# Kernel optimization log

Hardware: AMD Instinct MI355X
Metric: run time of the kernel (lower is better)

The kernel has to match this reference:

```python
import jax, jax.numpy as jnp
import numpy as np
from jax import lax

N, CI, CO, K, H, W_SP, M = 32, 256, 256, 3, 64, 64, 4
TAU = 1.0 / 30.0
PAD = 1  # spatial-preserving for k=3, stride=1, dilation=1


def setup_inputs() -> dict:
    key = jax.random.key(0)
    ks = jax.random.split(key, 6)
    # kaiming_normal fan_out for the kernel bank: fan_out = CO*K*K (per torch semantics on this 6D tensor layout)
    fan_out = CO * K * K
    std = np.sqrt(2.0 / fan_out)
    x = jax.random.normal(ks[0], (N, CI, H, W_SP), dtype=jnp.float32)
    Wbank = jax.random.normal(ks[1], (CO, M, CI, K, K), dtype=jnp.float32) * std
    Bbank = jnp.zeros((CO, M), dtype=jnp.float32)
    hid = CI // M  # att_fc hidden = in_channels // num_weights
    w1 = jax.random.normal(ks[2], (hid, CI), dtype=jnp.float32) * np.sqrt(1.0 / CI)
    b1 = jnp.zeros((hid,), dtype=jnp.float32)
    w2 = jax.random.normal(ks[3], (M, hid), dtype=jnp.float32) * np.sqrt(1.0 / hid)
    b2 = jnp.zeros((M,), dtype=jnp.float32)
    return {"x": x, "Wbank": Wbank, "Bbank": Bbank, "w1": w1, "b1": b1, "w2": w2, "b2": b2}


def reference(x, Wbank, Bbank, w1, b1, w2, b2):
    n, ci, h, w = x.shape
    co = Wbank.shape[0]
    # attention over kernels: global avg pool -> 1x1 conv MLP -> softmax(logits * tau)
    pooled = jnp.mean(x, axis=(2, 3))                      # N,Ci
    hmid = jax.nn.relu(pooled @ w1.T + b1)                 # N,hid
    logits = hmid @ w2.T + b2                              # N,M
    pi = jax.nn.softmax(logits * TAU, axis=1)              # N,M
    # per-sample aggregated kernels and biases
    wn = jnp.einsum("nm,omikl->noikl", pi, Wbank)          # N,Co,Ci,K,K
    bn = pi @ Bbank.T                                      # N,Co
    # batch-as-groups conv2d (spatial-preserving)
    xg = x.reshape(1, n * ci, h, w)
    wg = wn.reshape(n * co, ci, K, K)
    y = lax.conv_general_dilated(
        xg, wg,
        window_strides=(1, 1),
        padding=[(PAD, PAD), (PAD, PAD)],
        rhs_dilation=(1, 1),
        dimension_numbers=("NCHW", "OIHW", "NCHW"),
        feature_group_count=n,
    )
    y = y.reshape(n, co, h, w) + bn[:, :, None, None]
    return y
```

## Files before the change

kernel.cpp:

```cpp
#include <hip/hip_runtime.h>
#include <hip/hip_bf16.h>
#include <stdint.h>

typedef __bf16 bf16;
typedef __bf16 bf16x8 __attribute__((ext_vector_type(8)));
typedef float f32x4 __attribute__((ext_vector_type(4)));

#define TAU (1.0f/30.0f)

#define NB 32
#define CI 256
#define CO 256
#define HH 64
#define WW 64
#define HID 64

#define WN_ELEMS ((size_t)NB*8*9*16*512)
#define WN_BYTES (WN_ELEMS*2)
#define PLANE_E 34848
#define XB_ELEMS ((size_t)NB*32*PLANE_E)
#define XB_BYTES (XB_ELEMS*2)

__device__ __forceinline__ void async16(void* lds_uniform_base, const void* g_perlane) {
  __builtin_amdgcn_global_load_lds(
      (const __attribute__((address_space(1))) uint32_t*)g_perlane,
      (__attribute__((address_space(3))) uint32_t*)lds_uniform_base, 16, 0, 0);
}

__global__ void cvt_pool_kernel(const float* __restrict__ x, bf16* __restrict__ xb,
                                float* __restrict__ pooled) {
  const int cg = blockIdx.x, n = blockIdx.y, tid = threadIdx.x;
  const float* base = x + ((size_t)n*CI + cg*8)*4096;
  bf16* ob = xb + ((size_t)n*32 + cg)*PLANE_E;
  for (int i = tid; i < 260; i += 256) {
    int hr, wl;
    if (i < 66)       { hr = 0;       wl = i; }
    else if (i < 132) { hr = 65;      wl = i - 66; }
    else if (i < 196) { hr = i - 131; wl = 0; }
    else              { hr = i - 195; wl = 65; }
    *(int4*)(ob + ((size_t)hr*66 + wl)*8) = int4{0,0,0,0};
  }
  float s[8];
#pragma unroll
  for (int j = 0; j < 8; ++j) s[j] = 0.f;
  for (int it = 0; it < 16; ++it) {
    int pos = it*256 + tid;
    int h = pos >> 6, w = pos & 63;
    bf16x8 o;
#pragma unroll
    for (int j = 0; j < 8; ++j) {
      float v = base[(size_t)j*4096 + pos];
      s[j] += v;
      o[j] = (bf16)v;
    }
    *(bf16x8*)(ob + ((size_t)(h+1)*66 + (w+1))*8) = o;
  }
  __shared__ float red[4][8];
#pragma unroll
  for (int j = 0; j < 8; ++j)
#pragma unroll
    for (int off = 32; off; off >>= 1) s[j] += __shfl_xor(s[j], off);
  int wv = tid >> 6, lane = tid & 63;
  if (lane == 0)
#pragma unroll
    for (int j = 0; j < 8; ++j) red[wv][j] = s[j];
  __syncthreads();
  if (tid < 8) {
    float t = red[0][tid] + red[1][tid] + red[2][tid] + red[3][tid];
    pooled[n*CI + cg*8 + tid] = t * (1.0f/4096.0f);
  }
}

__global__ void attn_kernel(const float* __restrict__ pooled,
                            const float* __restrict__ w1, const float* __restrict__ b1,
                            const float* __restrict__ w2, const float* __restrict__ b2,
                            float* __restrict__ pi) {
  int n = blockIdx.x, h = threadIdx.x;
  __shared__ float hm[HID];
  __shared__ float lgs[4];
  const float* pr = pooled + n*CI;
  float s = b1[h];
  for (int c = 0; c < CI; ++c) s += pr[c] * w1[h*CI + c];
  hm[h] = s > 0.f ? s : 0.f;
  __syncthreads();
  if (h < 4) {
    float lg = b2[h];
    for (int k = 0; k < HID; ++k) lg += hm[k] * w2[h*HID + k];
    lgs[h] = lg * TAU;
  }
  __syncthreads();
  if (h == 0) {
    float mx = fmaxf(fmaxf(lgs[0], lgs[1]), fmaxf(lgs[2], lgs[3]));
    float e0 = expf(lgs[0]-mx), e1 = expf(lgs[1]-mx), e2 = expf(lgs[2]-mx), e3 = expf(lgs[3]-mx);
    float inv = 1.f / (e0+e1+e2+e3);
    pi[n*4+0] = e0*inv; pi[n*4+1] = e1*inv; pi[n*4+2] = e2*inv; pi[n*4+3] = e3*inv;
  }
}

__global__ void agg_kernel(const float* __restrict__ Wbank, const float* __restrict__ pi,
                           bf16* __restrict__ wn) {
  int wid = blockIdx.x * 4 + (threadIdx.x >> 6);
  int lane = threadIdx.x & 63;
  int c = wid / 144;
  int rem = wid - c*144;
  int kk = rem >> 4;
  int cbg = rem & 15;
  int co  = cbg*16 + (lane & 15);
  int ci0 = c*32 + (lane >> 4)*8;
  float w[4][8];
#pragma unroll
  for (int m = 0; m < 4; ++m)
#pragma unroll
    for (int j = 0; j < 8; ++j)
      w[m][j] = Wbank[(size_t)((co*4 + m)*256 + ci0 + j)*9 + kk];
  for (int n = 0; n < NB; ++n) {
    float p0 = pi[n*4+0], p1 = pi[n*4+1], p2 = pi[n*4+2], p3 = pi[n*4+3];
    bf16x8 o;
#pragma unroll
    for (int j = 0; j < 8; ++j)
      o[j] = (bf16)(p0*w[0][j] + p1*w[1][j] + p2*w[2][j] + p3*w[3][j]);
    *(bf16x8*)(wn + ((size_t)n*1152 + c*144 + kk*16 + cbg)*512 + lane*8) = o;
  }
}

#define WA_E (9*4*512)

#define LDG(st, rr, kxx, cc) { _Pragma("unroll") \
  for (int f = 0; f < 4; ++f) \
    S[st][f] = *(const bf16x8*)(xu + ((size_t)(cc)*139392 + (rr)*528 + f*128 + (kxx)*8)); }

#define MM(kkv, lo, hi) { \
  __builtin_amdgcn_s_setprio(1); \
  _Pragma("unroll") for (int cb = 0; cb < 4; ++cb) { \
    bf16x8 afr = *(const bf16x8*)(&wab[(kkv)*2048 + cb*512 + lane*8]); \
    _Pragma("unroll") for (int f = 0; f < 4; ++f) { \
      acc[0][cb][f] = __builtin_amdgcn_mfma_f32_16x16x32_bf16(afr, lo[f], acc[0][cb][f], 0,0,0); \
      acc[1][cb][f] = __builtin_amdgcn_mfma_f32_16x16x32_bf16(afr, hi[f], acc[1][cb][f], 0,0,0); \
    } } \
  __builtin_amdgcn_s_setprio(0); }

#define STAGE_W(cc, b) { const bf16* seg = wnb + (size_t)(cc)*73728; \
  _Pragma("unroll") for (int kk = 0; kk < 9; ++kk) \
    async16(&wa[b][kk*2048 + wv*512], seg + (size_t)kk*8192); }

__global__ __launch_bounds__(256, 2)
void conv_kernel(const bf16* __restrict__ xb, const bf16* __restrict__ wn,
                 const float* __restrict__ pi, const float* __restrict__ Bbank,
                 float* __restrict__ y) {
  __shared__ __align__(16) bf16 wa[2][WA_E];
  __shared__ float bns[64];
  const int tid = threadIdx.x;
  const int wv = tid >> 6, lane = tid & 63;
  const int l = lane & 15, u = lane >> 4;
  const int flat = blockIdx.x;
  const int wid = ((flat & 7) << 7) + (flat >> 3);
  const int n   = wid >> 5;
  const int hwb = (wid >> 2) & 7;
  const int cot = wid & 3;
  const int h0 = hwb * 8;

  const bf16* wnb = wn + (size_t)n*1152*512 + (size_t)(cot*4 + wv)*512 + lane*8;
  const bf16* xu = xb + (((size_t)(n*32 + u)*66 + (h0 + wv*2))*66 + l)*8;

  STAGE_W(0, 0);

  if (tid < 64) {
    int co = cot*64 + tid;
    bns[tid] = pi[n*4+0]*Bbank[co*4+0] + pi[n*4+1]*Bbank[co*4+1]
             + pi[n*4+2]*Bbank[co*4+2] + pi[n*4+3]*Bbank[co*4+3];
  }

  f32x4 acc[2][4][4];
#pragma unroll
  for (int o = 0; o < 2; ++o)
#pragma unroll
    for (int a = 0; a < 4; ++a)
#pragma unroll
      for (int b = 0; b < 4; ++b)
#pragma unroll
        for (int k = 0; k < 4; ++k) acc[o][a][b][k] = 0.f;

  for (int c = 0; c < 8; ++c) {
    __syncthreads();
    if (c < 7) STAGE_W(c + 1, (c + 1) & 1);
    const bf16* wab = wa[c & 1];
    bf16x8 S[4][4];
    LDG(0, 0, 0, c) LDG(1, 1, 0, c) LDG(2, 2, 0, c) LDG(3, 3, 0, c)
    MM(0, S[0], S[1])
    MM(3, S[1], S[2]) LDG(0, 0, 1, c) LDG(1, 1, 1, c)
    MM(6, S[2], S[3]) LDG(2, 2, 1, c)
    MM(1, S[0], S[1]) LDG(3, 3, 1, c)
    MM(4, S[1], S[2]) LDG(0, 0, 2, c) LDG(1, 1, 2, c)
    MM(7, S[2], S[3]) LDG(2, 2, 2, c)
    MM(2, S[0], S[1]) LDG(3, 3, 2, c)
    MM(5, S[1], S[2])
    MM(8, S[2], S[3])
  }
#pragma unroll
  for (int o = 0; o < 2; ++o) {
    const int h = h0 + wv*2 + o;
#pragma unroll
    for (int cb = 0; cb < 4; ++cb) {
#pragma unroll
      for (int f = 0; f < 4; ++f) {
        const int wcol = f*16 + l;
#pragma unroll
        for (int r4 = 0; r4 < 4; ++r4) {
          const int col = cb*16 + u*4 + r4;
          y[(((size_t)n*CO + cot*64 + col)*HH + h)*WW + wcol] = acc[o][cb][f][r4] + bns[col];
        }
      }
    }
  }
}

extern "C" void kernel_launch(void* const* d_in, const int* in_sizes, int n_in,
                              void* d_out, int out_size, void* d_ws, size_t ws_size,
                              hipStream_t stream) {
  const float* x     = (const float*)d_in[0];
  const float* Wbank = (const float*)d_in[1];
  const float* Bbank = (const float*)d_in[2];
  const float* w1    = (const float*)d_in[3];
  const float* b1    = (const float*)d_in[4];
  const float* w2    = (const float*)d_in[5];
  const float* b2    = (const float*)d_in[6];
  float* y = (float*)d_out;

  bf16*  wn     = (bf16*)d_ws;
  bf16*  xb     = (bf16*)((char*)d_ws + WN_BYTES);
  float* pooled = (float*)((char*)d_ws + WN_BYTES + XB_BYTES);
  float* pi     = pooled + NB*CI;

  dim3 cg(32, NB);
  cvt_pool_kernel<<<cg, 256, 0, stream>>>(x, xb, pooled);
  attn_kernel<<<NB, HID, 0, stream>>>(pooled, w1, b1, w2, b2, pi);
  agg_kernel<<<288, 256, 0, stream>>>(Wbank, pi, wn);
  conv_kernel<<<1024, 256, 0, stream>>>(xb, wn, pi, Bbank, y);
}
```

Measured before the change: 191.9 us.

## Switch conv MFMA to 32x32x16 tiles and prefetch next-chunk input rows

Replaces the 16x16x32 bf16 MFMA tiling with 32x32x16 instructions, reorganising the aggregated-weight layout in agg_kernel and the LDS staging to match the new A-fragment shape. The input B-fragments are reloaded with a new indexing that spans two channel groups per lane half. The first rows for the next channel chunk are prefetched during the last MFMAs of the current chunk. The aim is fewer MFMA issues and fewer fragment loads per FLOP, and to hide the global-load latency at chunk boundaries. The cost is more live registers, which puts pressure on the occupancy of 2 blocks per SIMD.

```diff
diff --git a/kernel.cpp b/kernel.cpp
--- a/kernel.cpp
+++ b/kernel.cpp
@@ -4,7 +4,7 @@
 
 typedef __bf16 bf16;
 typedef __bf16 bf16x8 __attribute__((ext_vector_type(8)));
-typedef float f32x4 __attribute__((ext_vector_type(4)));
+typedef float f32x16 __attribute__((ext_vector_type(16)));
 
 #define TAU (1.0f/30.0f)
 
@@ -15,7 +15,7 @@
 #define WW 64
 #define HID 64
 
-#define WN_ELEMS ((size_t)NB*8*9*16*512)
+#define WN_ELEMS ((size_t)NB*589824)
 #define WN_BYTES (WN_ELEMS*2)
 #define PLANE_E 34848
 #define XB_ELEMS ((size_t)NB*32*PLANE_E)
@@ -103,45 +103,50 @@
   int lane = threadIdx.x & 63;
   int c = wid / 144;
   int rem = wid - c*144;
-  int kk = rem >> 4;
-  int cbg = rem & 15;
-  int co  = cbg*16 + (lane & 15);
-  int ci0 = c*32 + (lane >> 4)*8;
+  int kk  = rem >> 4;
+  int r2  = rem & 15;
+  int cot = r2 >> 2;
+  int sub = (r2 >> 1) & 1;
+  int cbg = r2 & 1;
+  int co  = cot*64 + cbg*32 + (lane & 31);
+  int ci0 = c*32 + sub*16 + (lane >> 5)*8;
   float w[4][8];
 #pragma unroll
   for (int m = 0; m < 4; ++m)
 #pragma unroll
     for (int j = 0; j < 8; ++j)
       w[m][j] = Wbank[(size_t)((co*4 + m)*256 + ci0 + j)*9 + kk];
+  bf16* ob = wn + (size_t)c*73728 + (size_t)kk*8192 + cot*2048 + sub*1024 + cbg*512 + lane*8;
   for (int n = 0; n < NB; ++n) {
     float p0 = pi[n*4+0], p1 = pi[n*4+1], p2 = pi[n*4+2], p3 = pi[n*4+3];
     bf16x8 o;
 #pragma unroll
     for (int j = 0; j < 8; ++j)
       o[j] = (bf16)(p0*w[0][j] + p1*w[1][j] + p2*w[2][j] + p3*w[3][j]);
-    *(bf16x8*)(wn + ((size_t)n*1152 + c*144 + kk*16 + cbg)*512 + lane*8) = o;
-  }
-}
-
-#define WA_E (9*4*512)
-
-#define LDG(st, rr, kxx, cc) { _Pragma("unroll") \
-  for (int f = 0; f < 4; ++f) \
-    S[st][f] = *(const bf16x8*)(xu + ((size_t)(cc)*139392 + (rr)*528 + f*128 + (kxx)*8)); }
+    *(bf16x8*)(ob + (size_t)n*589824) = o;
+  }
+}
+
+#define WA_E (36*512)
+
+#define LDB(P, r, cc) { _Pragma("unroll") \
+  for (int sf = 0; sf < 4; ++sf) \
+    P[sf] = *(const bf16x8*)(xq + (size_t)((cc)*4 + (sf>>1)*2)*PLANE_E + (r)*528 + ((sf&1)*32 + kxv)*8); }
 
 #define MM(kkv, lo, hi) { \
   __builtin_amdgcn_s_setprio(1); \
-  _Pragma("unroll") for (int cb = 0; cb < 4; ++cb) { \
-    bf16x8 afr = *(const bf16x8*)(&wab[(kkv)*2048 + cb*512 + lane*8]); \
-    _Pragma("unroll") for (int f = 0; f < 4; ++f) { \
-      acc[0][cb][f] = __builtin_amdgcn_mfma_f32_16x16x32_bf16(afr, lo[f], acc[0][cb][f], 0,0,0); \
-      acc[1][cb][f] = __builtin_amdgcn_mfma_f32_16x16x32_bf16(afr, hi[f], acc[1][cb][f], 0,0,0); \
+  _Pragma("unroll") for (int sub = 0; sub < 2; ++sub) \
+  _Pragma("unroll") for (int cbg = 0; cbg < 2; ++cbg) { \
+    bf16x8 afr = *(const bf16x8*)(&wab[((kkv)*4 + sub*2 + cbg)*512 + lane*8]); \
+    _Pragma("unroll") for (int f = 0; f < 2; ++f) { \
+      acc[0][cbg][f] = __builtin_amdgcn_mfma_f32_32x32x16_bf16(afr, lo[sub*2+f], acc[0][cbg][f], 0,0,0); \
+      acc[1][cbg][f] = __builtin_amdgcn_mfma_f32_32x32x16_bf16(afr, hi[sub*2+f], acc[1][cbg][f], 0,0,0); \
     } } \
   __builtin_amdgcn_s_setprio(0); }
 
 #define STAGE_W(cc, b) { const bf16* seg = wnb + (size_t)(cc)*73728; \
-  _Pragma("unroll") for (int kk = 0; kk < 9; ++kk) \
-    async16(&wa[b][kk*2048 + wv*512], seg + (size_t)kk*8192); }
+  _Pragma("unroll") for (int i = 0; i < 9; ++i) { const int fid = i*4 + wv; \
+    async16(&wa[b][fid*512], seg + (size_t)(fid>>2)*8192 + (fid&3)*512); } }
 
 __global__ __launch_bounds__(256, 2)
 void conv_kernel(const bf16* __restrict__ xb, const bf16* __restrict__ wn,
@@ -151,7 +156,7 @@
   __shared__ float bns[64];
   const int tid = threadIdx.x;
   const int wv = tid >> 6, lane = tid & 63;
-  const int l = lane & 15, u = lane >> 4;
+  const int l = lane & 31, u = lane >> 5;
   const int flat = blockIdx.x;
   const int wid = ((flat & 7) << 7) + (flat >> 3);
   const int n   = wid >> 5;
@@ -159,9 +164,11 @@
   const int cot = wid & 3;
   const int h0 = hwb * 8;
 
-  const bf16* wnb = wn + (size_t)n*1152*512 + (size_t)(cot*4 + wv)*512 + lane*8;
-  const bf16* xu = xb + (((size_t)(n*32 + u)*66 + (h0 + wv*2))*66 + l)*8;
-
+  const bf16* wnb = wn + (size_t)n*589824 + cot*2048 + lane*8;
+  const bf16* xq = xb + (((size_t)(n*32 + u)*66 + (h0 + wv*2))*66 + l)*8;
+
+  bf16x8 S[4][4];
+  { const int kxv = 0; LDB(S[0], 0, 0) LDB(S[1], 1, 0) }
   STAGE_W(0, 0);
 
   if (tid < 64) {
@@ -170,44 +177,44 @@
              + pi[n*4+2]*Bbank[co*4+2] + pi[n*4+3]*Bbank[co*4+3];
   }
 
-  f32x4 acc[2][4][4];
+  f32x16 acc[2][2][2];
 #pragma unroll
   for (int o = 0; o < 2; ++o)
 #pragma unroll
-    for (int a = 0; a < 4; ++a)
-#pragma unroll
-      for (int b = 0; b < 4; ++b)
-#pragma unroll
-        for (int k = 0; k < 4; ++k) acc[o][a][b][k] = 0.f;
+    for (int a = 0; a < 2; ++a)
+#pragma unroll
+      for (int b = 0; b < 2; ++b)
+#pragma unroll
+        for (int k = 0; k < 16; ++k) acc[o][a][b][k] = 0.f;
 
   for (int c = 0; c < 8; ++c) {
     __syncthreads();
+    { const int kxv = 0; LDB(S[2], 2, c) LDB(S[3], 3, c) }
     if (c < 7) STAGE_W(c + 1, (c + 1) & 1);
     const bf16* wab = wa[c & 1];
-    bf16x8 S[4][4];
-    LDG(0, 0, 0, c) LDG(1, 1, 0, c) LDG(2, 2, 0, c) LDG(3, 3, 0, c)
+    const int cp = (c < 7) ? c + 1 : 7;
     MM(0, S[0], S[1])
-    MM(3, S[1], S[2]) LDG(0, 0, 1, c) LDG(1, 1, 1, c)
-    MM(6, S[2], S[3]) LDG(2, 2, 1, c)
-    MM(1, S[0], S[1]) LDG(3, 3, 1, c)
-    MM(4, S[1], S[2]) LDG(0, 0, 2, c) LDG(1, 1, 2, c)
-    MM(7, S[2], S[3]) LDG(2, 2, 2, c)
-    MM(2, S[0], S[1]) LDG(3, 3, 2, c)
-    MM(5, S[1], S[2])
+    MM(3, S[1], S[2]) { const int kxv = 1; LDB(S[0], 0, c) LDB(S[1], 1, c) }
+    MM(6, S[2], S[3]) { const int kxv = 1; LDB(S[2], 2, c) }
+    MM(1, S[0], S[1]) { const int kxv = 1; LDB(S[3], 3, c) }
+    MM(4, S[1], S[2]) { const int kxv = 2; LDB(S[0], 0, c) LDB(S[1], 1, c) }
+    MM(7, S[2], S[3]) { const int kxv = 2; LDB(S[2], 2, c) }
+    MM(2, S[0], S[1]) { const int kxv = 2; LDB(S[3], 3, c) }
+    MM(5, S[1], S[2]) { const int kxv = 0; LDB(S[0], 0, cp) LDB(S[1], 1, cp) }
     MM(8, S[2], S[3])
   }
 #pragma unroll
   for (int o = 0; o < 2; ++o) {
     const int h = h0 + wv*2 + o;
 #pragma unroll
-    for (int cb = 0; cb < 4; ++cb) {
-#pragma unroll
-      for (int f = 0; f < 4; ++f) {
-        const int wcol = f*16 + l;
-#pragma unroll
-        for (int r4 = 0; r4 < 4; ++r4) {
-          const int col = cb*16 + u*4 + r4;
-          y[(((size_t)n*CO + cot*64 + col)*HH + h)*WW + wcol] = acc[o][cb][f][r4] + bns[col];
+    for (int cbg = 0; cbg < 2; ++cbg) {
+#pragma unroll
+      for (int f = 0; f < 2; ++f) {
+        const int wcol = f*32 + l;
+#pragma unroll
+        for (int reg = 0; reg < 16; ++reg) {
+          const int col = cbg*32 + (reg & 3) + 8*(reg >> 2) + 4*u;
+          y[(((size_t)n*CO + cot*64 + col)*HH + h)*WW + wcol] = acc[o][cbg][f][reg] + bns[col];
         }
       }
     }
```

After: 208.1 us. +8.5%, slower.
